# Kernel tuning notes

Measured on AMD Instinct MI355X. Metric: run time of the kernel, lower is better.

## Reference

```python
import jax, jax.numpy as jnp
import numpy as np

SCALES = [3, 5, 7, 9]


def _conv1d(x, w, b, k):
    # x: (BN, 1, L), w: (1, 1, k), b: (1,) -> (BN, 1, L), 'same' padding (k//2)
    y = jax.lax.conv_general_dilated(
        x, w, window_strides=(1,), padding=[(k // 2, k // 2)],
        dimension_numbers=("NCH", "OIH", "NCH"))
    return y + b[None, :, None]


def setup_inputs() -> dict:
    key = jax.random.key(0)
    ks = jax.random.split(key, 16)
    B, N, L = 64, 321, 720
    inp = {"x": jax.random.normal(ks[0], (B, N, L), dtype=jnp.float32)}
    # Conv1d(1,1,k) params, kaiming-ish scale 1/sqrt(k)
    for i, s in enumerate(SCALES):
        inp[f"cw{i}"] = jax.random.normal(ks[1 + 2 * i], (1, 1, s), dtype=jnp.float32) / np.sqrt(s)
        inp[f"cb{i}"] = jax.random.normal(ks[2 + 2 * i], (1,), dtype=jnp.float32) * 0.01
    # weight_net: Linear(4,32) -> ReLU -> Linear(32,4) -> Softmax
    inp["W1"] = jax.random.normal(ks[10], (4, 32), dtype=jnp.float32) / np.sqrt(4.0)
    inp["b1"] = jnp.zeros((32,), dtype=jnp.float32)
    inp["W2"] = jax.random.normal(ks[11], (32, 4), dtype=jnp.float32) / np.sqrt(32.0)
    inp["b2"] = jnp.zeros((4,), dtype=jnp.float32)
    return inp


def reference(x, cw0, cb0, cw1, cb1, cw2, cb2, cw3, cb3, W1, b1, W2, b2):
    B, N, L = x.shape
    xf = x.reshape(B * N, 1, L)
    cparams = [(cw0, cb0), (cw1, cb1), (cw2, cb2), (cw3, cb3)]
    feats, ents = [], []
    for (w, b), k in zip(cparams, SCALES):
        f = _conv1d(xf, w, b, k)                      # (BN, 1, L)
        prob = jax.nn.softmax(f, axis=-1)
        ent = -(prob * jnp.log(prob + 1e-8)).sum(axis=-1)  # (BN, 1)
        feats.append(f)
        ents.append(ent)
    entropy_vec = jnp.concatenate(ents, axis=-1)      # (BN, 4)
    h = jax.nn.relu(entropy_vec @ W1 + b1)
    weights = jax.nn.softmax(h @ W2 + b2, axis=-1)    # (BN, 4)
    stacked = jnp.stack(feats, axis=1)                # (BN, 4, 1, L)
    trend = (stacked * weights[:, :, None, None]).sum(axis=1)  # (BN, 1, L)
    return trend.reshape(B, N, L)
```

## Files before the change

### kernel.cpp

```cpp
#include <hip/hip_runtime.h>
#include <math.h>

#define NT 64
#define L_LEN 720
#define NROWS (64 * 321)

#define LOG2E 1.4426950408889634f
#define LN2   0.6931471805599453f

template<int CTRL, int RM>
__device__ __forceinline__ float dpp_add(float x) {
    int t = __builtin_amdgcn_update_dpp(0, __float_as_int(x), CTRL, RM, 0xf, true);
    return x + __int_as_float(t);
}

__device__ __forceinline__ float wave_sum64(float x) {
    x = dpp_add<0x111, 0xf>(x);
    x = dpp_add<0x112, 0xf>(x);
    x = dpp_add<0x114, 0xf>(x);
    x = dpp_add<0x118, 0xf>(x);
    x = dpp_add<0x142, 0xa>(x);
    x = dpp_add<0x143, 0xc>(x);
    return __int_as_float(__builtin_amdgcn_readlane(__float_as_int(x), 63));
}

__device__ __forceinline__ float half_sum32(float x) {
    x = dpp_add<0x111, 0xf>(x);
    x = dpp_add<0x112, 0xf>(x);
    x = dpp_add<0x114, 0xf>(x);
    x = dpp_add<0x118, 0xf>(x);
    x = dpp_add<0x142, 0xa>(x);
    return __int_as_float(__builtin_amdgcn_readlane(__float_as_int(x), 31));
}

__global__ __launch_bounds__(NT, 4) void trend_kernel(
    const float* __restrict__ x,
    const float* __restrict__ cw0, const float* __restrict__ cb0,
    const float* __restrict__ cw1, const float* __restrict__ cb1,
    const float* __restrict__ cw2, const float* __restrict__ cb2,
    const float* __restrict__ cw3, const float* __restrict__ cb3,
    const float* __restrict__ W1, const float* __restrict__ b1,
    const float* __restrict__ W2, const float* __restrict__ b2,
    float* __restrict__ out)
{
    const int lane = threadIdx.x;
    const int row  = blockIdx.x;

    const float* __restrict__ xr = x + (size_t)row * L_LEN;

    const int ll = (lane < 60) ? lane : 59;
    const int e0 = 12 * ll - 4;
    float xw[20];
#pragma unroll
    for (int q = 0; q < 5; ++q) {
        int e = e0 + 4 * q;
        e = (e < 0) ? 0 : ((e > L_LEN - 4) ? (L_LEN - 4) : e);
        float4 v = *(const float4*)(xr + e);
        xw[4 * q + 0] = v.x; xw[4 * q + 1] = v.y;
        xw[4 * q + 2] = v.z; xw[4 * q + 3] = v.w;
    }

    const float* cws[4] = {cw0, cw1, cw2, cw3};
    const float* cbs[4] = {cb0, cb1, cb2, cb3};
    float w2[4][9], bs2[4];
#pragma unroll
    for (int s = 0; s < 4; ++s) {
        const int k = 3 + 2 * s;
        bs2[s] = cbs[s][0] * LOG2E;
#pragma unroll
        for (int t = 0; t < 9; ++t)
            w2[s][t] = (t < k) ? (cws[s][t] * LOG2E) : 0.0f;
    }

    if (lane == 0)  { xw[0] = 0.f; xw[1] = 0.f; xw[2] = 0.f; xw[3] = 0.f; }
    if (lane == 59) { xw[16] = 0.f; xw[17] = 0.f; xw[18] = 0.f; xw[19] = 0.f; }

#pragma unroll
    for (int t = 0; t < 20; ++t) asm volatile("" : "+v"(xw[t]));

    float S[4]  = {0.f, 0.f, 0.f, 0.f};
    float Tu[4] = {0.f, 0.f, 0.f, 0.f};
#pragma unroll
    for (int e = 0; e < 12; ++e) {
#pragma unroll
        for (int s = 0; s < 4; ++s) {
            const int k = 3 + 2 * s;
            const int off = 3 - s;
            float u = bs2[s];
#pragma unroll
            for (int t = 0; t < k; ++t)
                u = fmaf(w2[s][t], xw[e + off + t], u);
            float ev = __builtin_amdgcn_exp2f(u);
            S[s]  += ev;
            Tu[s]  = fmaf(u, ev, Tu[s]);
        }
    }

    const bool active = lane < 60;
#pragma unroll
    for (int s = 0; s < 4; ++s) {
        S[s]  = active ? S[s]  : 0.0f;
        Tu[s] = active ? Tu[s] : 0.0f;
    }

    float ent[4];
#pragma unroll
    for (int s = 0; s < 4; ++s) {
        float Sg = wave_sum64(S[s]);
        float Tg = wave_sum64(Tu[s]);
        ent[s] = LN2 * (__builtin_amdgcn_logf(Sg)
                        - Tg * __builtin_amdgcn_rcpf(Sg));
    }

    const int hidx = lane & 31;
    float h = b1[hidx];
#pragma unroll
    for (int s = 0; s < 4; ++s) h = fmaf(ent[s], W1[s * 32 + hidx], h);
    h = fmaxf(h, 0.0f);

    const float4 w2v = ((const float4*)W2)[hidx];
    float lg[4];
    lg[0] = half_sum32(h * w2v.x) + b2[0];
    lg[1] = half_sum32(h * w2v.y) + b2[1];
    lg[2] = half_sum32(h * w2v.z) + b2[2];
    lg[3] = half_sum32(h * w2v.w) + b2[3];

    float m = fmaxf(fmaxf(lg[0], lg[1]), fmaxf(lg[2], lg[3]));
    float e0w = __expf(lg[0] - m), e1w = __expf(lg[1] - m);
    float e2w = __expf(lg[2] - m), e3w = __expf(lg[3] - m);
    float inv = LN2 / (e0w + e1w + e2w + e3w);
    const float wgt[4] = {e0w * inv, e1w * inv, e2w * inv, e3w * inv};

    float Wm[9] = {0,0,0,0,0,0,0,0,0};
    float Bm = 0.f;
#pragma unroll
    for (int s = 0; s < 4; ++s) {
        const int k = 3 + 2 * s;
        const int off = 3 - s;
#pragma unroll
        for (int t = 0; t < k; ++t)
            Wm[off + t] = fmaf(wgt[s], w2[s][t], Wm[off + t]);
        Bm = fmaf(wgt[s], bs2[s], Bm);
    }

    if (active) {
        float* __restrict__ orow = out + (size_t)row * L_LEN + 12 * lane;
#pragma unroll
        for (int q = 0; q < 3; ++q) {
            float4 v;
#pragma unroll
            for (int c = 0; c < 4; ++c) {
                const int e = 4 * q + c;
                float acc = Bm;
#pragma unroll
                for (int j = 0; j < 9; ++j)
                    acc = fmaf(Wm[j], xw[e + j], acc);
                ((float*)&v)[c] = acc;
            }
            *(float4*)(orow + 4 * q) = v;
        }
    }
}

extern "C" void kernel_launch(void* const* d_in, const int* in_sizes, int n_in,
                              void* d_out, int out_size, void* d_ws, size_t ws_size,
                              hipStream_t stream) {
    const float* xp  = (const float*)d_in[0];
    const float* cw0 = (const float*)d_in[1];
    const float* cb0 = (const float*)d_in[2];
    const float* cw1 = (const float*)d_in[3];
    const float* cb1 = (const float*)d_in[4];
    const float* cw2 = (const float*)d_in[5];
    const float* cb2 = (const float*)d_in[6];
    const float* cw3 = (const float*)d_in[7];
    const float* cb3 = (const float*)d_in[8];
    const float* W1  = (const float*)d_in[9];
    const float* b1  = (const float*)d_in[10];
    const float* W2  = (const float*)d_in[11];
    const float* b2  = (const float*)d_in[12];
    float* outp = (float*)d_out;

    trend_kernel<<<NROWS, NT, 0, stream>>>(xp, cw0, cb0, cw1, cb1, cw2, cb2,
                                           cw3, cb3, W1, b1, W2, b2, outp);
}
```

Measured before the change: 37.37 us.

## Process four rows per wave with double-buffered row prefetch

Each 64-thread block now handles four consecutive rows instead of one. It keeps two register windows so the next row's input loads are issued while the current row is being computed. Conv weights and MLP parameters are loaded once per block and reused across the four rows, which amortises setup and hides global load latency. The trade-offs are a 4x smaller grid (5136 blocks) and higher register pressure from the second 20-float window, which could lower occupancy.

After: 42.60 us. 1.14x slower.

```diff
diff --git a/kernel.cpp b/kernel.cpp
--- a/kernel.cpp
+++ b/kernel.cpp
@@ -4,6 +4,8 @@
 #define NT 64
 #define L_LEN 720
 #define NROWS (64 * 321)
+#define RPW 4
+#define NBLK (NROWS / RPW)
 
 #define LOG2E 1.4426950408889634f
 #define LN2   0.6931471805599453f
@@ -31,6 +33,18 @@
     x = dpp_add<0x118, 0xf>(x);
     x = dpp_add<0x142, 0xa>(x);
     return __int_as_float(__builtin_amdgcn_readlane(__float_as_int(x), 31));
+}
+
+__device__ __forceinline__ void load_win(const float* __restrict__ xr, int e0,
+                                         float (&xw)[20]) {
+#pragma unroll
+    for (int q = 0; q < 5; ++q) {
+        int e = e0 + 4 * q;
+        e = (e < 0) ? 0 : ((e > L_LEN - 4) ? (L_LEN - 4) : e);
+        float4 v = *(const float4*)(xr + e);
+        xw[4 * q + 0] = v.x; xw[4 * q + 1] = v.y;
+        xw[4 * q + 2] = v.z; xw[4 * q + 3] = v.w;
+    }
 }
 
 __global__ __launch_bounds__(NT, 4) void trend_kernel(
@@ -44,21 +58,16 @@
     float* __restrict__ out)
 {
     const int lane = threadIdx.x;
-    const int row  = blockIdx.x;
-
-    const float* __restrict__ xr = x + (size_t)row * L_LEN;
+    const int row0 = blockIdx.x * RPW;
 
     const int ll = (lane < 60) ? lane : 59;
     const int e0 = 12 * ll - 4;
-    float xw[20];
-#pragma unroll
-    for (int q = 0; q < 5; ++q) {
-        int e = e0 + 4 * q;
-        e = (e < 0) ? 0 : ((e > L_LEN - 4) ? (L_LEN - 4) : e);
-        float4 v = *(const float4*)(xr + e);
-        xw[4 * q + 0] = v.x; xw[4 * q + 1] = v.y;
-        xw[4 * q + 2] = v.z; xw[4 * q + 3] = v.w;
-    }
+    const bool active = lane < 60;
+
+    const float* __restrict__ xr0 = x + (size_t)row0 * L_LEN;
+    float xwA[20], xwB[20];
+    load_win(xr0, e0, xwA);
+    load_win(xr0 + L_LEN, e0, xwB);
 
     const float* cws[4] = {cw0, cw1, cw2, cw3};
     const float* cbs[4] = {cb0, cb1, cb2, cb3};
@@ -71,95 +80,105 @@
         for (int t = 0; t < 9; ++t)
             w2[s][t] = (t < k) ? (cws[s][t] * LOG2E) : 0.0f;
     }
-
-    if (lane == 0)  { xw[0] = 0.f; xw[1] = 0.f; xw[2] = 0.f; xw[3] = 0.f; }
-    if (lane == 59) { xw[16] = 0.f; xw[17] = 0.f; xw[18] = 0.f; xw[19] = 0.f; }
-
-#pragma unroll
-    for (int t = 0; t < 20; ++t) asm volatile("" : "+v"(xw[t]));
-
-    float S[4]  = {0.f, 0.f, 0.f, 0.f};
-    float Tu[4] = {0.f, 0.f, 0.f, 0.f};
-#pragma unroll
-    for (int e = 0; e < 12; ++e) {
+    const int hidx = lane & 31;
+    float w1r[4];
+#pragma unroll
+    for (int s = 0; s < 4; ++s) w1r[s] = W1[s * 32 + hidx];
+    const float b1r = b1[hidx];
+    const float4 w2r = ((const float4*)W2)[hidx];
+    const float b20 = b2[0], b21 = b2[1], b22 = b2[2], b23 = b2[3];
+
+    auto compute = [&](float (&xw)[20], int row) {
+#pragma unroll
+        for (int t = 0; t < 20; ++t) asm volatile("" : "+v"(xw[t]));
+        if (lane == 0)  { xw[0] = 0.f; xw[1] = 0.f; xw[2] = 0.f; xw[3] = 0.f; }
+        if (lane == 59) { xw[16] = 0.f; xw[17] = 0.f; xw[18] = 0.f; xw[19] = 0.f; }
+
+        float S[4]  = {0.f, 0.f, 0.f, 0.f};
+        float Tu[4] = {0.f, 0.f, 0.f, 0.f};
+#pragma unroll
+        for (int e = 0; e < 12; ++e) {
+#pragma unroll
+            for (int s = 0; s < 4; ++s) {
+                const int k = 3 + 2 * s;
+                const int off = 3 - s;
+                float u = bs2[s];
+#pragma unroll
+                for (int t = 0; t < k; ++t)
+                    u = fmaf(w2[s][t], xw[e + off + t], u);
+                float ev = __builtin_amdgcn_exp2f(u);
+                S[s]  += ev;
+                Tu[s]  = fmaf(u, ev, Tu[s]);
+            }
+        }
+#pragma unroll
+        for (int s = 0; s < 4; ++s) {
+            S[s]  = active ? S[s]  : 0.0f;
+            Tu[s] = active ? Tu[s] : 0.0f;
+        }
+
+        float ent[4];
+#pragma unroll
+        for (int s = 0; s < 4; ++s) {
+            float Sg = wave_sum64(S[s]);
+            float Tg = wave_sum64(Tu[s]);
+            ent[s] = LN2 * (__builtin_amdgcn_logf(Sg)
+                            - Tg * __builtin_amdgcn_rcpf(Sg));
+        }
+
+        float h = b1r;
+#pragma unroll
+        for (int s = 0; s < 4; ++s) h = fmaf(ent[s], w1r[s], h);
+        h = fmaxf(h, 0.0f);
+
+        float lg0 = half_sum32(h * w2r.x) + b20;
+        float lg1 = half_sum32(h * w2r.y) + b21;
+        float lg2 = half_sum32(h * w2r.z) + b22;
+        float lg3 = half_sum32(h * w2r.w) + b23;
+
+        float m = fmaxf(fmaxf(lg0, lg1), fmaxf(lg2, lg3));
+        float e0w = __expf(lg0 - m), e1w = __expf(lg1 - m);
+        float e2w = __expf(lg2 - m), e3w = __expf(lg3 - m);
+        float inv = LN2 / (e0w + e1w + e2w + e3w);
+        const float wgt[4] = {e0w * inv, e1w * inv, e2w * inv, e3w * inv};
+
+        float Wm[9] = {0,0,0,0,0,0,0,0,0};
+        float Bm = 0.f;
 #pragma unroll
         for (int s = 0; s < 4; ++s) {
             const int k = 3 + 2 * s;
             const int off = 3 - s;
-            float u = bs2[s];
 #pragma unroll
             for (int t = 0; t < k; ++t)
-                u = fmaf(w2[s][t], xw[e + off + t], u);
-            float ev = __builtin_amdgcn_exp2f(u);
-            S[s]  += ev;
-            Tu[s]  = fmaf(u, ev, Tu[s]);
-        }
-    }
-
-    const bool active = lane < 60;
-#pragma unroll
-    for (int s = 0; s < 4; ++s) {
-        S[s]  = active ? S[s]  : 0.0f;
-        Tu[s] = active ? Tu[s] : 0.0f;
-    }
-
-    float ent[4];
-#pragma unroll
-    for (int s = 0; s < 4; ++s) {
-        float Sg = wave_sum64(S[s]);
-        float Tg = wave_sum64(Tu[s]);
-        ent[s] = LN2 * (__builtin_amdgcn_logf(Sg)
-                        - Tg * __builtin_amdgcn_rcpf(Sg));
-    }
-
-    const int hidx = lane & 31;
-    float h = b1[hidx];
-#pragma unroll
-    for (int s = 0; s < 4; ++s) h = fmaf(ent[s], W1[s * 32 + hidx], h);
-    h = fmaxf(h, 0.0f);
-
-    const float4 w2v = ((const float4*)W2)[hidx];
-    float lg[4];
-    lg[0] = half_sum32(h * w2v.x) + b2[0];
-    lg[1] = half_sum32(h * w2v.y) + b2[1];
-    lg[2] = half_sum32(h * w2v.z) + b2[2];
-    lg[3] = half_sum32(h * w2v.w) + b2[3];
-
-    float m = fmaxf(fmaxf(lg[0], lg[1]), fmaxf(lg[2], lg[3]));
-    float e0w = __expf(lg[0] - m), e1w = __expf(lg[1] - m);
-    float e2w = __expf(lg[2] - m), e3w = __expf(lg[3] - m);
-    float inv = LN2 / (e0w + e1w + e2w + e3w);
-    const float wgt[4] = {e0w * inv, e1w * inv, e2w * inv, e3w * inv};
-
-    float Wm[9] = {0,0,0,0,0,0,0,0,0};
-    float Bm = 0.f;
-#pragma unroll
-    for (int s = 0; s < 4; ++s) {
-        const int k = 3 + 2 * s;
-        const int off = 3 - s;
-#pragma unroll
-        for (int t = 0; t < k; ++t)
-            Wm[off + t] = fmaf(wgt[s], w2[s][t], Wm[off + t]);
-        Bm = fmaf(wgt[s], bs2[s], Bm);
-    }
-
-    if (active) {
-        float* __restrict__ orow = out + (size_t)row * L_LEN + 12 * lane;
-#pragma unroll
-        for (int q = 0; q < 3; ++q) {
-            float4 v;
-#pragma unroll
-            for (int c = 0; c < 4; ++c) {
-                const int e = 4 * q + c;
-                float acc = Bm;
-#pragma unroll
-                for (int j = 0; j < 9; ++j)
-                    acc = fmaf(Wm[j], xw[e + j], acc);
-                ((float*)&v)[c] = acc;
+                Wm[off + t] = fmaf(wgt[s], w2[s][t], Wm[off + t]);
+            Bm = fmaf(wgt[s], bs2[s], Bm);
+        }
+
+        if (active) {
+            float* __restrict__ orow = out + (size_t)row * L_LEN + 12 * lane;
+#pragma unroll
+            for (int q = 0; q < 3; ++q) {
+                float4 v;
+#pragma unroll
+                for (int c = 0; c < 4; ++c) {
+                    const int e = 4 * q + c;
+                    float acc = Bm;
+#pragma unroll
+                    for (int j = 0; j < 9; ++j)
+                        acc = fmaf(Wm[j], xw[e + j], acc);
+                    ((float*)&v)[c] = acc;
+                }
+                *(float4*)(orow + 4 * q) = v;
             }
-            *(float4*)(orow + 4 * q) = v;
-        }
-    }
+        }
+    };
+
+    compute(xwA, row0 + 0);
+    load_win(xr0 + 2 * L_LEN, e0, xwA);
+    compute(xwB, row0 + 1);
+    load_win(xr0 + 3 * L_LEN, e0, xwB);
+    compute(xwA, row0 + 2);
+    compute(xwB, row0 + 3);
 }
 
 extern "C" void kernel_launch(void* const* d_in, const int* in_sizes, int n_in,
@@ -180,6 +199,6 @@
     const float* b2  = (const float*)d_in[12];
     float* outp = (float*)d_out;
 
-    trend_kernel<<<NROWS, NT, 0, stream>>>(xp, cw0, cb0, cw1, cb1, cw2, cb2,
-                                           cw3, cb3, W1, b1, W2, b2, outp);
-}
+    trend_kernel<<<NBLK, NT, 0, stream>>>(xp, cw0, cb0, cw1, cb1, cw2, cb2,
+                                          cw3, cb3, W1, b1, W2, b2, outp);
+}
```
